# Kernel optimization log

Measured on AMD Instinct MI355X. Metric: run time of the kernel, lower is better.

The kernel has to match this reference:

```python
import jax, jax.numpy as jnp
import numpy as np

G, B, K, D = 16384, 4, 2, 64
NEG = -1e30


def _mlp3(x, w1, b1, w2, b2, w3, b3):
    # MLP: linear->relu x3 (BatchNorm defined but unused in original forward)
    h = jax.nn.relu(x @ w1 + b1)
    h = jax.nn.relu(h @ w2 + b2)
    return jax.nn.relu(h @ w3 + b3)


def setup_inputs() -> dict:
    key = jax.random.key(0)
    ks = jax.random.split(key, 32)

    def lin(k, fan_in, fan_out):
        k1, k2 = jax.random.split(k)
        s = 1.0 / np.sqrt(fan_in)
        w = jax.random.uniform(k1, (fan_in, fan_out), jnp.float32, -s, s)
        b = jax.random.uniform(k2, (fan_out,), jnp.float32, -s, s)
        return w, b

    inp = {}
    inp['ap_feat'] = jax.random.normal(ks[0], (G, B, 1), jnp.float32)
    inp['e_feat'] = jax.random.normal(ks[1], (G, B, K, 2), jnp.float32)
    inp['w_pre_ap'], inp['b_pre_ap'] = lin(ks[2], 1, D)
    inp['w_pre_edge'], inp['b_pre_edge'] = lin(ks[3], 2, D)
    # mlp_update_5 (AP-side neighbor messages), _6 (UE-side), _7 (edge update)
    inp['w5_1'], inp['b5_1'] = lin(ks[4], 2 * D, D)
    inp['w5_2'], inp['b5_2'] = lin(ks[5], D, D)
    inp['w5_3'], inp['b5_3'] = lin(ks[6], D, D)
    inp['w6_1'], inp['b6_1'] = lin(ks[7], 2 * D, D)
    inp['w6_2'], inp['b6_2'] = lin(ks[8], D, D)
    inp['w6_3'], inp['b6_3'] = lin(ks[9], D, D)
    inp['w7_1'], inp['b7_1'] = lin(ks[10], 2 * D, D)
    inp['w7_2'], inp['b7_2'] = lin(ks[11], D, D)
    inp['w7_3'], inp['b7_3'] = lin(ks[12], D, D)
    inp['w_post'], inp['b_post'] = lin(ks[13], D, 2)
    return inp


def _edge_conv(e, a, w5_1, b5_1, w5_2, b5_2, w5_3, b5_3,
               w6_1, b6_1, w6_2, b6_2, w6_3, b6_3,
               w7_1, b7_1, w7_2, b7_2, w7_3, b7_3):
    # e: [G,B,K,D] AP2UE edge hid; a: [G,B,D] AP hid.
    # M1[g,b,j] = mlp5(cat(a[g,b], e[g,b,j])) -- same-AP neighbor edges
    x1 = jnp.concatenate([jnp.broadcast_to(a[:, :, None, :], e.shape), e], axis=-1)  # [G,B,K,2D]
    M1 = _mlp3(x1, w5_1, b5_1, w5_2, b5_2, w5_3, b5_3)  # [G,B,K,D]
    # M2[g,b,bp,k] = mlp6(cat(a[g,b], e[g,bp,k])) -- same-UE neighbor edges
    # (original uses the SRC AP feature here too). Split first linear to
    # avoid materializing the [G,B,B,K,2D] concat.
    h = jax.nn.relu(
        (a @ w6_1[:D])[:, :, None, None, :]
        + (e @ w6_1[D:])[:, None, :, :, :]
        + b6_1)  # [G,B,B,K,D]
    h = jax.nn.relu(h @ w6_2 + b6_2)
    M2 = jax.nn.relu(h @ w6_3 + b6_3)  # [G,B,Bp,K,D]
    # masked max excluding the edge itself
    eyeK = jnp.eye(K, dtype=bool)  # [k, j]
    m1max = jnp.max(jnp.where(eyeK[None, None, :, :, None], NEG,
                              M1[:, :, None, :, :]), axis=3)  # [G,B,K,D]
    eyeB = jnp.eye(B, dtype=bool)  # [b, bp]
    m2max = jnp.max(jnp.where(eyeB[None, :, :, None, None], NEG, M2), axis=2)  # [G,B,K,D]
    agg = jnp.maximum(m1max, m2max)
    # new edge feature: mlp7(cat(agg, e_hid))
    return _mlp3(jnp.concatenate([agg, e], axis=-1),
                 w7_1, b7_1, w7_2, b7_2, w7_3, b7_3)


def reference(ap_feat, e_feat, w_pre_ap, b_pre_ap, w_pre_edge, b_pre_edge,
              w5_1, b5_1, w5_2, b5_2, w5_3, b5_3,
              w6_1, b6_1, w6_2, b6_2, w6_3, b6_3,
              w7_1, b7_1, w7_2, b7_2, w7_3, b7_3,
              w_post, b_post):
    # PreLayer (live branches only: AP nodes and AP2UE edges; APConv/UEConv
    # write node 'new' which is never read, so UE/UE2AP branches are dead).
    a = jax.nn.relu(ap_feat @ w_pre_ap + b_pre_ap)   # [G,B,D]
    e = jax.nn.relu(e_feat @ w_pre_edge + b_pre_edge)  # [G,B,K,D]
    # two UpdateLayers (shared weights: ModuleList([UpdateLayer()]*2) + global MLPs)
    for _ in range(2):
        e = _edge_conv(e, a, w5_1, b5_1, w5_2, b5_2, w5_3, b5_3,
                       w6_1, b6_1, w6_2, b6_2, w6_3, b6_3,
                       w7_1, b7_1, w7_2, b7_2, w7_3, b7_3)
    out = e @ w_post + b_post  # [G,B,K,2]
    r, im = out[..., 0], out[..., 1]
    # norm_func: per-graph [B,K] complex matrix, each row (over K) L2-normalized
    n = jnp.sqrt(jnp.sum(r * r + im * im, axis=-1, keepdims=True))
    return jnp.stack([r / n, im / n], axis=-1)  # [G,B,K,2]
```

## Files before the change

kernel.cpp:

```cpp
#include <hip/hip_runtime.h>


typedef unsigned short u16;
typedef unsigned int   u32;
typedef __attribute__((ext_vector_type(8))) short short8_t;
typedef __attribute__((ext_vector_type(2))) short short2v;
typedef __attribute__((ext_vector_type(4))) float floatx4;

#define LDSFENCE() asm volatile("" ::: "memory")

#define OFF_W51 0
#define OFF_W61 8192
#define OFF_W71 16384
#define OFF_W52 24576
#define OFF_W53 28672
#define OFF_W62 32768
#define OFF_W63 36864
#define OFF_W72 40960
#define OFF_W73 45056
#define WS_U16  49152

#define CB51 0
#define CB52 64
#define CB53 128
#define CB61 192
#define CB62 256
#define CB63 320
#define CB71 384
#define CB72 448
#define CB73 512
#define CWPO 576
#define CBPO 704
#define CWPA 768
#define CBPA 832
#define CWPE 896
#define CBPE 1024
#define CSZ  1088

#define BUF_U16 1088
#define APB_U16 544
#define PW_U16  3264

struct Params {
  const float *ap, *ef;
  const float *wpa, *bpa, *wpe, *bpe;
  const float *w51, *b51, *w52, *b52, *w53, *b53;
  const float *w61, *b61, *w62, *b62, *w63, *b63;
  const float *w71, *b71, *w72, *b72, *w73, *b73;
  const float *wpost, *bpost;
  float *out;
  int gtot;
};

__device__ __forceinline__ u32 pk2(float a, float b) {
  const u32 ua = __float_as_uint(a) + 0x8000u;
  const u32 ub = __float_as_uint(b) + 0x8000u;
  return __builtin_amdgcn_perm(ub, ua, 0x07060302u);
}
__device__ __forceinline__ float blo(u32 v) { return __uint_as_float(v << 16); }
__device__ __forceinline__ float bhi(u32 v) { return __uint_as_float(v & 0xffff0000u); }
__device__ __forceinline__ u32 pkmax(u32 a, u32 b) {
  const short2v r = __builtin_elementwise_max(__builtin_bit_cast(short2v, a),
                                              __builtin_bit_cast(short2v, b));
  return __builtin_bit_cast(u32, r);
}
__device__ __forceinline__ float sel4(int i, float x0, float x1, float x2, float x3) {
  const float lo = (i & 1) ? x1 : x0;
  const float hi = (i & 1) ? x3 : x2;
  return (i & 2) ? hi : lo;
}

__device__ __forceinline__ floatx4 mfma16(short8_t a, short8_t b, floatx4 c) {
  return __builtin_amdgcn_mfma_f32_16x16x32_bf16(a, b, c, 0, 0, 0);
}
__device__ __forceinline__ int rowN(int row) { return row * 8 + (row >> 4) * 8; }
__device__ __forceinline__ short8_t ldN(const u16* buf, int row) {
  const uint4 v = *(const uint4*)(buf + rowN(row));
  return __builtin_bit_cast(short8_t, v);
}
__device__ __forceinline__ uint4 ldN4(const u16* buf, int row) {
  return *(const uint4*)(buf + rowN(row));
}

template<int TSTRIDE>
__device__ __forceinline__ void layerK64R2(floatx4* aX, floatx4* aY,
                                           short8_t x0, short8_t x1,
                                           short8_t y0, short8_t y1,
                                           const u16* B, int l) {
#pragma unroll
  for (int t = 0; t < 4; ++t) {
    const short8_t b0 = *(const short8_t*)(B + (t * TSTRIDE + 0) * 512 + l * 8);
    const short8_t b1 = *(const short8_t*)(B + (t * TSTRIDE + 1) * 512 + l * 8);
    aX[t] = mfma16(x0, b0, aX[t]);
    aY[t] = mfma16(y0, b0, aY[t]);
    aX[t] = mfma16(x1, b1, aX[t]);
    aY[t] = mfma16(y1, b1, aY[t]);
  }
}

__device__ __forceinline__ void layerK128R2(floatx4* aX, floatx4* aY,
                                            const short8_t* fx, const short8_t* fy,
                                            const u16* B, int l) {
#pragma unroll
  for (int t = 0; t < 4; ++t)
#pragma unroll
    for (int h = 0; h < 4; ++h) {
      const short8_t b = *(const short8_t*)(B + (t * 4 + h) * 512 + l * 8);
      aX[t] = mfma16(fx[h], b, aX[t]);
      aY[t] = mfma16(fy[h], b, aY[t]);
    }
}

__device__ __forceinline__ void scatterN_relu(u16* dst, const floatx4* acc, int q, int n) {
  u32* d32 = (u32*)dst;
  const int g = n >> 2, d = n & 3;
#pragma unroll
  for (int tp = 0; tp < 2; ++tp)
#pragma unroll
    for (int r = 0; r < 4; ++r) {
      const int row = tp * 64 + g * 16 + 4 * q + r;
      d32[row * 4 + (row >> 4) * 4 + d] =
          pkmax(pk2(acc[2 * tp + 0][r], acc[2 * tp + 1][r]), 0u);
    }
  LDSFENCE();
}
__device__ __forceinline__ void scatterN_raw(u16* dst, const floatx4* acc, int q, int n) {
  u32* d32 = (u32*)dst;
  const int g = n >> 2, d = n & 3;
#pragma unroll
  for (int tp = 0; tp < 2; ++tp)
#pragma unroll
    for (int r = 0; r < 4; ++r) {
      const int row = tp * 64 + g * 16 + 4 * q + r;
      d32[row * 4 + (row >> 4) * 4 + d] = pk2(acc[2 * tp + 0][r], acc[2 * tp + 1][r]);
    }
  LDSFENCE();
}
__device__ __forceinline__ void scatterN_u32(u16* dst, const u32* v, int q, int n) {
  u32* d32 = (u32*)dst;
  const int g = n >> 2, d = n & 3;
#pragma unroll
  for (int tp = 0; tp < 2; ++tp)
#pragma unroll
    for (int r = 0; r < 4; ++r) {
      const int row = tp * 64 + g * 16 + 4 * q + r;
      d32[row * 4 + (row >> 4) * 4 + d] = v[tp * 4 + r];
    }
  LDSFENCE();
}

__device__ __forceinline__ void scatter_aP(u16* dst, const floatx4* acc, int q, int n,
                                           const float* cb61) {
  u32* d32 = (u32*)dst;
  const int g = n >> 2, d = n & 3;
#pragma unroll
  for (int tp = 0; tp < 2; ++tp) {
    const float bv0 = cb61[32 * tp + n];
    const float bv1 = cb61[32 * tp + 16 + n];
#pragma unroll
    for (int rh = 0; rh < 2; ++rh) {
      const int row = tp * 32 + g * 8 + 2 * q + rh;
      d32[row * 4 + (row >> 4) * 4 + d] =
          pk2(acc[2 * tp + 0][2 * rh] + bv0, acc[2 * tp + 1][2 * rh] + bv1);
    }
  }
  LDSFENCE();
}

__device__ __forceinline__ void init_accL(floatx4* acc, const float* cb, int n) {
#pragma unroll
  for (int t = 0; t < 4; ++t) {
    const float b = cb[16 * t + n];
    floatx4 v; v[0] = b; v[1] = b; v[2] = b; v[3] = b;
    acc[t] = v;
  }
}
__device__ __forceinline__ void init_acc0(floatx4* acc) {
#pragma unroll
  for (int t = 0; t < 4; ++t) { acc[t][0] = 0.f; acc[t][1] = 0.f; acc[t][2] = 0.f; acc[t][3] = 0.f; }
}

struct frag2 { short8_t f0, f1; };

__device__ __forceinline__ frag2 make_a(float apv, int q, const float* sc) {
  frag2 r;
#pragma unroll
  for (int h = 0; h < 2; ++h) {
    const int fb = 32 * h + 8 * q;
    const float4 wa0 = *(const float4*)(sc + CWPA + fb);
    const float4 wa1 = *(const float4*)(sc + CWPA + fb + 4);
    const float4 ba0 = *(const float4*)(sc + CBPA + fb);
    const float4 ba1 = *(const float4*)(sc + CBPA + fb + 4);
    uint4 pa;
    pa.x = pk2(fmaxf(fmaf(apv, wa0.x, ba0.x), 0.f), fmaxf(fmaf(apv, wa0.y, ba0.y), 0.f));
    pa.y = pk2(fmaxf(fmaf(apv, wa0.z, ba0.z), 0.f), fmaxf(fmaf(apv, wa0.w, ba0.w), 0.f));
    pa.z = pk2(fmaxf(fmaf(apv, wa1.x, ba1.x), 0.f), fmaxf(fmaf(apv, wa1.y, ba1.y), 0.f));
    pa.w = pk2(fmaxf(fmaf(apv, wa1.z, ba1.z), 0.f), fmaxf(fmaf(apv, wa1.w, ba1.w), 0.f));
    if (h == 0) r.f0 = __builtin_bit_cast(short8_t, pa);
    else        r.f1 = __builtin_bit_cast(short8_t, pa);
  }
  return r;
}

__device__ __forceinline__ void prelayer(frag2& A, short8_t& e0, short8_t& e1,
                                         const Params& p, const float* sc,
                                         int g0, int q, int n) {
  const float apv = p.ap[(g0 + (n >> 3)) * 4 + ((n >> 1) & 3)];
  A = make_a(apv, q, sc);
  const float f0 = p.ef[(g0 + (n >> 3)) * 16 + (n & 7) * 2];
  const float f1 = p.ef[(g0 + (n >> 3)) * 16 + (n & 7) * 2 + 1];
#pragma unroll
  for (int h = 0; h < 2; ++h) {
    const int fb = 32 * h + 8 * q;
    const float4 w00 = *(const float4*)(sc + CWPE + fb);
    const float4 w01 = *(const float4*)(sc + CWPE + fb + 4);
    const float4 w10 = *(const float4*)(sc + CWPE + 64 + fb);
    const float4 w11 = *(const float4*)(sc + CWPE + 64 + fb + 4);
    const float4 be0 = *(const float4*)(sc + CBPE + fb);
    const float4 be1 = *(const float4*)(sc + CBPE + fb + 4);
    uint4 pe;
    pe.x = pk2(fmaxf(fmaf(f0, w00.x, fmaf(f1, w10.x, be0.x)), 0.f),
               fmaxf(fmaf(f0, w00.y, fmaf(f1, w10.y, be0.y)), 0.f));
    pe.y = pk2(fmaxf(fmaf(f0, w00.z, fmaf(f1, w10.z, be0.z)), 0.f),
               fmaxf(fmaf(f0, w00.w, fmaf(f1, w10.w, be0.w)), 0.f));
    pe.z = pk2(fmaxf(fmaf(f0, w01.x, fmaf(f1, w11.x, be1.x)), 0.f),
               fmaxf(fmaf(f0, w01.y, fmaf(f1, w11.y, be1.y)), 0.f));
    pe.w = pk2(fmaxf(fmaf(f0, w01.z, fmaf(f1, w11.z, be1.z)), 0.f),
               fmaxf(fmaf(f0, w01.w, fmaf(f1, w11.w, be1.w)), 0.f));
    if (h == 0) e0 = __builtin_bit_cast(short8_t, pe);
    else        e1 = __builtin_bit_cast(short8_t, pe);
  }
}

__device__ __forceinline__ void build_h(short8_t* hf0, short8_t* hf1,
                                        const u16* aPb, const u16* BUF,
                                        int q, int n) {
  const int b_ln = (n >> 1) & 3;
  const int ar = 8 * q + (n >> 1);
  const uint4 av0 = ldN4(aPb, ar);
  const uint4 av1 = ldN4(aPb, 32 + ar);
#pragma unroll
  for (int j = 0; j < 3; ++j) {
    const int bp = j + (j >= b_ln);
    const int re = (n & 8) + bp * 2 + (n & 1);
    const uint4 ev0 = ldN4(BUF, 16 * q + re);
    const uint4 ev1 = ldN4(BUF, 64 + 16 * q + re);
    uint4 p0, p1;
    p0.x = pk2(fmaxf(blo(av0.x) + blo(ev0.x), 0.f), fmaxf(bhi(av0.x) + bhi(ev0.x), 0.f));
    p0.y = pk2(fmaxf(blo(av0.y) + blo(ev0.y), 0.f), fmaxf(bhi(av0.y) + bhi(ev0.y), 0.f));
    p0.z = pk2(fmaxf(blo(av0.z) + blo(ev0.z), 0.f), fmaxf(bhi(av0.z) + bhi(ev0.z), 0.f));
    p0.w = pk2(fmaxf(blo(av0.w) + blo(ev0.w), 0.f), fmaxf(bhi(av0.w) + bhi(ev0.w), 0.f));
    p1.x = pk2(fmaxf(blo(av1.x) + blo(ev1.x), 0.f), fmaxf(bhi(av1.x) + bhi(ev1.x), 0.f));
    p1.y = pk2(fmaxf(blo(av1.y) + blo(ev1.y), 0.f), fmaxf(bhi(av1.y) + bhi(ev1.y), 0.f));
    p1.z = pk2(fmaxf(blo(av1.z) + blo(ev1.z), 0.f), fmaxf(bhi(av1.z) + bhi(ev1.z), 0.f));
    p1.w = pk2(fmaxf(blo(av1.w) + blo(ev1.w), 0.f), fmaxf(bhi(av1.w) + bhi(ev1.w), 0.f));
    hf0[j] = __builtin_bit_cast(short8_t, p0);
    hf1[j] = __builtin_bit_cast(short8_t, p1);
  }
}

__device__ __forceinline__ void epilogue(const floatx4* acc3, const float* sc,
                                         float* out, int g0, int q, int n, bool ok) {
  float prr[4] = {0.f, 0.f, 0.f, 0.f}, pii[4] = {0.f, 0.f, 0.f, 0.f};
#pragma unroll
  for (int t = 0; t < 4; ++t) {
    const float wr = sc[CWPO + (16 * t + n) * 2];
    const float wi = sc[CWPO + (16 * t + n) * 2 + 1];
#pragma unroll
    for (int r = 0; r < 4; ++r) {
      const float e = fmaxf(acc3[t][r], 0.f);
      prr[r] = fmaf(e, wr, prr[r]);
      pii[r] = fmaf(e, wi, pii[r]);
    }
  }
  const float bpR = sc[CBPO], bpI = sc[CBPO + 1];
#pragma unroll
  for (int r = 0; r < 4; ++r) {
#pragma unroll
    for (int off = 1; off < 16; off <<= 1) {
      prr[r] += __shfl_xor(prr[r], off, 16);
      pii[r] += __shfl_xor(pii[r], off, 16);
    }
    prr[r] += bpR;
    pii[r] += bpI;
  }
  const int r = n >> 1, c = n & 1, rp = r ^ 1;
  const float pr_r  = sel4(r,  prr[0], prr[1], prr[2], prr[3]);
  const float pi_r  = sel4(r,  pii[0], pii[1], pii[2], pii[3]);
  const float pr_rp = sel4(rp, prr[0], prr[1], prr[2], prr[3]);
  const float pi_rp = sel4(rp, pii[0], pii[1], pii[2], pii[3]);
  const float num = c ? pi_r : pr_r;
  const float n2  = pr_r * pr_r + pi_r * pi_r + pr_rp * pr_rp + pi_rp * pi_rp;
  if (ok && n < 8) out[g0 * 16 + (4 * q + r) * 2 + c] = num / sqrtf(n2);
}

#define NBLK 256
#define NWAVE 8
#define PPW  2

__global__ __launch_bounds__(512, 2)
__attribute__((amdgpu_waves_per_eu(2, 2)))
void hetgnn_mfma(Params p) {
  __shared__ __align__(16) u16   sW[WS_U16];
  __shared__ __align__(16) u16   sAct[NWAVE * PW_U16];
  __shared__ __align__(16) float sConst[CSZ];

  const int tid  = threadIdx.x;
  const int wave = tid >> 6;
  const int l    = tid & 63;
  const int q    = l >> 4;
  const int n    = l & 15;

  {
    for (int fi = wave; fi < 96; fi += NWAVE) {
      int t, h, mi;
      if (fi < 48) { mi = fi >> 4; const int loc = fi & 15; t = loc >> 2; h = loc & 3; }
      else { const int j = fi - 48; mi = 3 + (j >> 3); const int loc = j & 7; t = loc >> 1; h = loc & 1; }
      const float* W =
          (mi == 0) ? p.w51 : (mi == 1) ? p.w61 : (mi == 2) ? p.w71 :
          (mi == 3) ? p.w52 : (mi == 4) ? p.w53 : (mi == 5) ? p.w62 :
          (mi == 6) ? p.w63 : (mi == 7) ? p.w72 : p.w73;
      const int nn = 16 * t + n;
      float w[8];
#pragma unroll
      for (int jj = 0; jj < 8; ++jj) {
        const int kidx = (fi < 48)
            ? 64 * (h >> 1) + 32 * (h & 1) + (jj & 1) * 16 + 4 * q + (jj >> 1)
            : 32 * h + (jj & 1) * 16 + 4 * q + (jj >> 1);
        w[jj] = W[kidx * 64 + nn];
      }
      uint4 o;
      o.x = pk2(w[0], w[1]); o.y = pk2(w[2], w[3]);
      o.z = pk2(w[4], w[5]); o.w = pk2(w[6], w[7]);
      *(uint4*)(sW + fi * 512 + l * 8) = o;
    }
  }
  if (tid < 64) {
    sConst[CB51 + tid] = p.b51[tid];
    sConst[CB52 + tid] = p.b52[tid];
    sConst[CB53 + tid] = p.b53[tid];
    sConst[CB61 + tid] = p.b61[tid];
    sConst[CB62 + tid] = p.b62[tid];
    sConst[CB63 + tid] = p.b63[tid];
    sConst[CB71 + tid] = p.b71[tid];
    sConst[CB72 + tid] = p.b72[tid];
    sConst[CB73 + tid] = p.b73[tid];
    const int feat = 32 * (tid >> 5) + (tid & 1) * 16 + 4 * ((tid >> 3) & 3) + ((tid >> 1) & 3);
    sConst[CWPA + tid] = p.wpa[feat];
    sConst[CBPA + tid] = p.bpa[feat];
    sConst[CBPE + tid] = p.bpe[feat];
  }
  if (tid < 128) {
    sConst[CWPO + tid] = p.wpost[tid];
    const int s = tid & 63;
    const int feat = 32 * (s >> 5) + (s & 1) * 16 + 4 * ((s >> 3) & 3) + ((s >> 1) & 3);
    sConst[CWPE + tid] = p.wpe[(tid >> 6) * 64 + feat];
  }
  if (tid < 2) sConst[CBPO + tid] = p.bpost[tid];
  __syncthreads();

  u16* BUF0 = sAct + wave * PW_U16;
  u16* aPb0 = BUF0 + BUF_U16;
  u16* BUF1 = aPb0 + APB_U16;
  u16* aPb1 = BUF1 + BUF_U16;

  const int wslot = blockIdx.x * NWAVE + wave;

#pragma unroll 1
  for (int pi = 0; pi < PPW; ++pi) {
    const int g0X = (wslot * 4 + 2 * pi) * 2;
    const int g0Y = g0X + 2;
    if (g0X + 2 > p.gtot) break;
    const bool okY = (g0Y + 2 <= p.gtot);
    const int gY  = okY ? g0Y : g0X;

    frag2 AX, AY;
    short8_t ex0, ex1, ey0, ey1;
    prelayer(AX, ex0, ex1, p, sConst, g0X, q, n);
    prelayer(AY, ey0, ey1, p, sConst, gY,  q, n);

    {
      floatx4 aaX[4], aaY[4];
      init_acc0(aaX); init_acc0(aaY);
      layerK64R2<4>(aaX, aaY, AX.f0, AX.f1, AY.f0, AY.f1, sW + OFF_W61, l);
      scatter_aP(aPb0, aaX, q, n, sConst + CB61);
      scatter_aP(aPb1, aaY, q, n, sConst + CB61);
    }

#pragma unroll 1
    for (int it = 0; it < 2; ++it) {
      if (it == 1) {
        ex0 = ldN(BUF0, l); ex1 = ldN(BUF0, 64 + l);
        ey0 = ldN(BUF1, l); ey1 = ldN(BUF1, 64 + l);
      }

      u32 m1pX[8], m1pY[8];
      {
        floatx4 aX[4], aY[4];
        init_accL(aX, sConst + CB51, n); init_accL(aY, sConst + CB51, n);
        const short8_t fx[4] = {AX.f0, AX.f1, ex0, ex1};
        const short8_t fy[4] = {AY.f0, AY.f1, ey0, ey1};
        layerK128R2(aX, aY, fx, fy, sW + OFF_W51, l);
        scatterN_relu(BUF0, aX, q, n);
        scatterN_relu(BUF1, aY, q, n);
        floatx4 bX[4], bY[4];
        init_accL(bX, sConst + CB52, n); init_accL(bY, sConst + CB52, n);
        {
          const short8_t gx0 = ldN(BUF0, l), gx1 = ldN(BUF0, 64 + l);
          const short8_t gy0 = ldN(BUF1, l), gy1 = ldN(BUF1, 64 + l);
          layerK64R2<2>(bX, bY, gx0, gx1, gy0, gy1, sW + OFF_W52, l);
        }
        scatterN_relu(BUF0, bX, q, n);
        scatterN_relu(BUF1, bY, q, n);
        floatx4 cX[4], cY[4];
        init_accL(cX, sConst + CB53, n); init_accL(cY, sConst + CB53, n);
        {
          const short8_t gx0 = ldN(BUF0, l), gx1 = ldN(BUF0, 64 + l);
          const short8_t gy0 = ldN(BUF1, l), gy1 = ldN(BUF1, 64 + l);
          layerK64R2<2>(cX, cY, gx0, gx1, gy0, gy1, sW + OFF_W53, l);
        }
#pragma unroll
        for (int tp = 0; tp < 2; ++tp)
#pragma unroll
          for (int r = 0; r < 4; ++r) {
            m1pX[tp * 4 + r] = pk2(cX[2 * tp][r], cX[2 * tp + 1][r]);
            m1pY[tp * 4 + r] = pk2(cY[2 * tp][r], cY[2 * tp + 1][r]);
          }
      }

      u32 m2pX[8], m2pY[8];
      {
        floatx4 eX[4], eY[4];
        init_acc0(eX); init_acc0(eY);
        layerK64R2<4>(eX, eY, ex0, ex1, ey0, ey1, sW + OFF_W61 + 2 * 512, l);
        scatterN_raw(BUF0, eX, q, n);
        scatterN_raw(BUF1, eY, q, n);

        short8_t hfX0[3], hfX1[3], hfY0[3], hfY1[3];
        build_h(hfX0, hfX1, aPb0, BUF0, q, n);
        build_h(hfY0, hfY1, aPb1, BUF1, q, n);

#pragma unroll
        for (int j = 0; j < 3; ++j) {
          floatx4 uX[4], uY[4];
          init_accL(uX, sConst + CB62, n); init_accL(uY, sConst + CB62, n);
          layerK64R2<2>(uX, uY, hfX0[j], hfX1[j], hfY0[j], hfY1[j], sW + OFF_W62, l);
          scatterN_relu(BUF0, uX, q, n);
          scatterN_relu(BUF1, uY, q, n);
          floatx4 vX[4], vY[4];
          init_accL(vX, sConst + CB63, n); init_accL(vY, sConst + CB63, n);
          {
            const short8_t gx0 = ldN(BUF0, l), gx1 = ldN(BUF0, 64 + l);
            const short8_t gy0 = ldN(BUF1, l), gy1 = ldN(BUF1, 64 + l);
            layerK64R2<2>(vX, vY, gx0, gx1, gy0, gy1, sW + OFF_W63, l);
          }
#pragma unroll
          for (int tp = 0; tp < 2; ++tp)
#pragma unroll
            for (int r = 0; r < 4; ++r) {
              const u32 cXv = pk2(vX[2 * tp][r], vX[2 * tp + 1][r]);
              const u32 cYv = pk2(vY[2 * tp][r], vY[2 * tp + 1][r]);
              const int i = tp * 4 + r;
              m2pX[i] = (j == 0) ? cXv : pkmax(m2pX[i], cXv);
              m2pY[i] = (j == 0) ? cYv : pkmax(m2pY[i], cYv);
            }
        }
      }

      {
        u32 agX[8], agY[8];
#pragma unroll
        for (int tp = 0; tp < 2; ++tp)
#pragma unroll
          for (int r = 0; r < 4; ++r) {
            const int i = tp * 4 + r;
            agX[i] = pkmax(pkmax(m1pX[tp * 4 + (r ^ 1)], m2pX[i]), 0u);
            agY[i] = pkmax(pkmax(m1pY[tp * 4 + (r ^ 1)], m2pY[i]), 0u);
          }
        scatterN_u32(BUF0, agX, q, n);
        scatterN_u32(BUF1, agY, q, n);
        floatx4 aX[4], aY[4];
        init_accL(aX, sConst + CB71, n); init_accL(aY, sConst + CB71, n);
        {
          const short8_t gx0 = ldN(BUF0, l), gx1 = ldN(BUF0, 64 + l);
          const short8_t gy0 = ldN(BUF1, l), gy1 = ldN(BUF1, 64 + l);
          const short8_t fx[4] = {gx0, gx1, ex0, ex1};
          const short8_t fy[4] = {gy0, gy1, ey0, ey1};
          layerK128R2(aX, aY, fx, fy, sW + OFF_W71, l);
        }
        scatterN_relu(BUF0, aX, q, n);
        scatterN_relu(BUF1, aY, q, n);
        floatx4 bX[4], bY[4];
        init_accL(bX, sConst + CB72, n); init_accL(bY, sConst + CB72, n);
        {
          const short8_t gx0 = ldN(BUF0, l), gx1 = ldN(BUF0, 64 + l);
          const short8_t gy0 = ldN(BUF1, l), gy1 = ldN(BUF1, 64 + l);
          layerK64R2<2>(bX, bY, gx0, gx1, gy0, gy1, sW + OFF_W72, l);
        }
        scatterN_relu(BUF0, bX, q, n);
        scatterN_relu(BUF1, bY, q, n);
        floatx4 cX[4], cY[4];
        init_accL(cX, sConst + CB73, n); init_accL(cY, sConst + CB73, n);
        {
          const short8_t gx0 = ldN(BUF0, l), gx1 = ldN(BUF0, 64 + l);
          const short8_t gy0 = ldN(BUF1, l), gy1 = ldN(BUF1, 64 + l);
          layerK64R2<2>(cX, cY, gx0, gx1, gy0, gy1, sW + OFF_W73, l);
        }

        if (it == 0) {
          scatterN_relu(BUF0, cX, q, n);
          scatterN_relu(BUF1, cY, q, n);
        } else {
          epilogue(cX, sConst, p.out, g0X, q, n, true);
          epilogue(cY, sConst, p.out, g0Y, q, n, okY);
        }
      }
    }
  }
}

extern "C" void kernel_launch(void* const* d_in, const int* in_sizes, int n_in,
                              void* d_out, int out_size, void* d_ws, size_t ws_size,
                              hipStream_t stream) {
  Params p;
  p.ap    = (const float*)d_in[0];
  p.ef    = (const float*)d_in[1];
  p.wpa   = (const float*)d_in[2];  p.bpa   = (const float*)d_in[3];
  p.wpe   = (const float*)d_in[4];  p.bpe   = (const float*)d_in[5];
  p.w51   = (const float*)d_in[6];  p.b51   = (const float*)d_in[7];
  p.w52   = (const float*)d_in[8];  p.b52   = (const float*)d_in[9];
  p.w53   = (const float*)d_in[10]; p.b53   = (const float*)d_in[11];
  p.w61   = (const float*)d_in[12]; p.b61   = (const float*)d_in[13];
  p.w62   = (const float*)d_in[14]; p.b62   = (const float*)d_in[15];
  p.w63   = (const float*)d_in[16]; p.b63   = (const float*)d_in[17];
  p.w71   = (const float*)d_in[18]; p.b71   = (const float*)d_in[19];
  p.w72   = (const float*)d_in[20]; p.b72   = (const float*)d_in[21];
  p.w73   = (const float*)d_in[22]; p.b73   = (const float*)d_in[23];
  p.wpost = (const float*)d_in[24]; p.bpost = (const float*)d_in[25];
  p.out   = (float*)d_out;
  p.gtot  = in_sizes[0] / 4;

  hipLaunchKernelGGL(hetgnn_mfma, dim3(NBLK), dim3(512), 0, stream, p);
}
```

Measured before the change: 149.8 us.

## Drop split-linear mlp6 trick and dual-tile interleave for one tile per wave

The wave now handles one 2-graph tile per pass instead of two interleaved X/Y tiles, with four passes per wave instead of two. The precomputed a@W61 and e@W61 halves and the VALU-built relu(a+e) hidden fragments are removed. Each of the three mlp6 neighbours now runs a full K=128 MFMA over the concatenated [a, e_neighbour] read from an LDS edge buffer. This trades more matrix work for less VALU bf16 unpack/add work, fewer live registers and less LDS per wave, but it loses the instruction-level parallelism that two independent tiles gave.

```diff
diff --git a/kernel.cpp b/kernel.cpp
--- a/kernel.cpp
+++ b/kernel.cpp
@@ -38,8 +38,8 @@
 #define CSZ  1088
 
 #define BUF_U16 1088
-#define APB_U16 544
-#define PW_U16  3264
+#define ET_U16  1088
+#define PW_U16  2176
 
 struct Params {
   const float *ap, *ef;
@@ -57,8 +57,6 @@
   const u32 ub = __float_as_uint(b) + 0x8000u;
   return __builtin_amdgcn_perm(ub, ua, 0x07060302u);
 }
-__device__ __forceinline__ float blo(u32 v) { return __uint_as_float(v << 16); }
-__device__ __forceinline__ float bhi(u32 v) { return __uint_as_float(v & 0xffff0000u); }
 __device__ __forceinline__ u32 pkmax(u32 a, u32 b) {
   const short2v r = __builtin_elementwise_max(__builtin_bit_cast(short2v, a),
                                               __builtin_bit_cast(short2v, b));
@@ -78,37 +76,31 @@
   const uint4 v = *(const uint4*)(buf + rowN(row));
   return __builtin_bit_cast(short8_t, v);
 }
-__device__ __forceinline__ uint4 ldN4(const u16* buf, int row) {
-  return *(const uint4*)(buf + rowN(row));
-}
-
-template<int TSTRIDE>
-__device__ __forceinline__ void layerK64R2(floatx4* aX, floatx4* aY,
+__device__ __forceinline__ void writeF(u16* buf, int row, short8_t f) {
+  *(uint4*)(buf + rowN(row)) = __builtin_bit_cast(uint4, f);
+}
+
+template<int TS>
+__device__ __forceinline__ void layerK64R(floatx4* acc, short8_t x0, short8_t x1,
+                                          const u16* B, int l) {
+#pragma unroll
+  for (int t = 0; t < 4; ++t) {
+    const short8_t b0 = *(const short8_t*)(B + (t * TS + 0) * 512 + l * 8);
+    const short8_t b1 = *(const short8_t*)(B + (t * TS + 1) * 512 + l * 8);
+    acc[t] = mfma16(x0, b0, acc[t]);
+    acc[t] = mfma16(x1, b1, acc[t]);
+  }
+}
+__device__ __forceinline__ void layerK128R(floatx4* acc,
                                            short8_t x0, short8_t x1,
-                                           short8_t y0, short8_t y1,
+                                           short8_t x2, short8_t x3,
                                            const u16* B, int l) {
-#pragma unroll
-  for (int t = 0; t < 4; ++t) {
-    const short8_t b0 = *(const short8_t*)(B + (t * TSTRIDE + 0) * 512 + l * 8);
-    const short8_t b1 = *(const short8_t*)(B + (t * TSTRIDE + 1) * 512 + l * 8);
-    aX[t] = mfma16(x0, b0, aX[t]);
-    aY[t] = mfma16(y0, b0, aY[t]);
-    aX[t] = mfma16(x1, b1, aX[t]);
-    aY[t] = mfma16(y1, b1, aY[t]);
-  }
-}
-
-__device__ __forceinline__ void layerK128R2(floatx4* aX, floatx4* aY,
-                                            const short8_t* fx, const short8_t* fy,
-                                            const u16* B, int l) {
+  const short8_t x[4] = {x0, x1, x2, x3};
 #pragma unroll
   for (int t = 0; t < 4; ++t)
 #pragma unroll
-    for (int h = 0; h < 4; ++h) {
-      const short8_t b = *(const short8_t*)(B + (t * 4 + h) * 512 + l * 8);
-      aX[t] = mfma16(fx[h], b, aX[t]);
-      aY[t] = mfma16(fy[h], b, aY[t]);
-    }
+    for (int h = 0; h < 4; ++h)
+      acc[t] = mfma16(x[h], *(const short8_t*)(B + (t * 4 + h) * 512 + l * 8), acc[t]);
 }
 
 __device__ __forceinline__ void scatterN_relu(u16* dst, const floatx4* acc, int q, int n) {
@@ -124,18 +116,6 @@
     }
   LDSFENCE();
 }
-__device__ __forceinline__ void scatterN_raw(u16* dst, const floatx4* acc, int q, int n) {
-  u32* d32 = (u32*)dst;
-  const int g = n >> 2, d = n & 3;
-#pragma unroll
-  for (int tp = 0; tp < 2; ++tp)
-#pragma unroll
-    for (int r = 0; r < 4; ++r) {
-      const int row = tp * 64 + g * 16 + 4 * q + r;
-      d32[row * 4 + (row >> 4) * 4 + d] = pk2(acc[2 * tp + 0][r], acc[2 * tp + 1][r]);
-    }
-  LDSFENCE();
-}
 __device__ __forceinline__ void scatterN_u32(u16* dst, const u32* v, int q, int n) {
   u32* d32 = (u32*)dst;
   const int g = n >> 2, d = n & 3;
@@ -146,24 +126,6 @@
       const int row = tp * 64 + g * 16 + 4 * q + r;
       d32[row * 4 + (row >> 4) * 4 + d] = v[tp * 4 + r];
     }
-  LDSFENCE();
-}
-
-__device__ __forceinline__ void scatter_aP(u16* dst, const floatx4* acc, int q, int n,
-                                           const float* cb61) {
-  u32* d32 = (u32*)dst;
-  const int g = n >> 2, d = n & 3;
-#pragma unroll
-  for (int tp = 0; tp < 2; ++tp) {
-    const float bv0 = cb61[32 * tp + n];
-    const float bv1 = cb61[32 * tp + 16 + n];
-#pragma unroll
-    for (int rh = 0; rh < 2; ++rh) {
-      const int row = tp * 32 + g * 8 + 2 * q + rh;
-      d32[row * 4 + (row >> 4) * 4 + d] =
-          pk2(acc[2 * tp + 0][2 * rh] + bv0, acc[2 * tp + 1][2 * rh] + bv1);
-    }
-  }
   LDSFENCE();
 }
 
@@ -174,10 +136,6 @@
     floatx4 v; v[0] = b; v[1] = b; v[2] = b; v[3] = b;
     acc[t] = v;
   }
-}
-__device__ __forceinline__ void init_acc0(floatx4* acc) {
-#pragma unroll
-  for (int t = 0; t < 4; ++t) { acc[t][0] = 0.f; acc[t][1] = 0.f; acc[t][2] = 0.f; acc[t][3] = 0.f; }
 }
 
 struct frag2 { short8_t f0, f1; };
@@ -232,35 +190,8 @@
   }
 }
 
-__device__ __forceinline__ void build_h(short8_t* hf0, short8_t* hf1,
-                                        const u16* aPb, const u16* BUF,
-                                        int q, int n) {
-  const int b_ln = (n >> 1) & 3;
-  const int ar = 8 * q + (n >> 1);
-  const uint4 av0 = ldN4(aPb, ar);
-  const uint4 av1 = ldN4(aPb, 32 + ar);
-#pragma unroll
-  for (int j = 0; j < 3; ++j) {
-    const int bp = j + (j >= b_ln);
-    const int re = (n & 8) + bp * 2 + (n & 1);
-    const uint4 ev0 = ldN4(BUF, 16 * q + re);
-    const uint4 ev1 = ldN4(BUF, 64 + 16 * q + re);
-    uint4 p0, p1;
-    p0.x = pk2(fmaxf(blo(av0.x) + blo(ev0.x), 0.f), fmaxf(bhi(av0.x) + bhi(ev0.x), 0.f));
-    p0.y = pk2(fmaxf(blo(av0.y) + blo(ev0.y), 0.f), fmaxf(bhi(av0.y) + bhi(ev0.y), 0.f));
-    p0.z = pk2(fmaxf(blo(av0.z) + blo(ev0.z), 0.f), fmaxf(bhi(av0.z) + bhi(ev0.z), 0.f));
-    p0.w = pk2(fmaxf(blo(av0.w) + blo(ev0.w), 0.f), fmaxf(bhi(av0.w) + bhi(ev0.w), 0.f));
-    p1.x = pk2(fmaxf(blo(av1.x) + blo(ev1.x), 0.f), fmaxf(bhi(av1.x) + bhi(ev1.x), 0.f));
-    p1.y = pk2(fmaxf(blo(av1.y) + blo(ev1.y), 0.f), fmaxf(bhi(av1.y) + bhi(ev1.y), 0.f));
-    p1.z = pk2(fmaxf(blo(av1.z) + blo(ev1.z), 0.f), fmaxf(bhi(av1.z) + bhi(ev1.z), 0.f));
-    p1.w = pk2(fmaxf(blo(av1.w) + blo(ev1.w), 0.f), fmaxf(bhi(av1.w) + bhi(ev1.w), 0.f));
-    hf0[j] = __builtin_bit_cast(short8_t, p0);
-    hf1[j] = __builtin_bit_cast(short8_t, p1);
-  }
-}
-
 __device__ __forceinline__ void epilogue(const floatx4* acc3, const float* sc,
-                                         float* out, int g0, int q, int n, bool ok) {
+                                         float* out, int g0, int q, int n) {
   float prr[4] = {0.f, 0.f, 0.f, 0.f}, pii[4] = {0.f, 0.f, 0.f, 0.f};
 #pragma unroll
   for (int t = 0; t < 4; ++t) {
@@ -291,12 +222,12 @@
   const float pi_rp = sel4(rp, pii[0], pii[1], pii[2], pii[3]);
   const float num = c ? pi_r : pr_r;
   const float n2  = pr_r * pr_r + pi_r * pi_r + pr_rp * pr_rp + pi_rp * pi_rp;
-  if (ok && n < 8) out[g0 * 16 + (4 * q + r) * 2 + c] = num / sqrtf(n2);
+  if (n < 8) out[g0 * 16 + (4 * q + r) * 2 + c] = num / sqrtf(n2);
 }
 
 #define NBLK 256
 #define NWAVE 8
-#define PPW  2
+#define PPW  4
 
 __global__ __launch_bounds__(512, 2)
 __attribute__((amdgpu_waves_per_eu(2, 2)))
@@ -359,160 +290,108 @@
   if (tid < 2) sConst[CBPO + tid] = p.bpost[tid];
   __syncthreads();
 
-  u16* BUF0 = sAct + wave * PW_U16;
-  u16* aPb0 = BUF0 + BUF_U16;
-  u16* BUF1 = aPb0 + APB_U16;
-  u16* aPb1 = BUF1 + BUF_U16;
+  u16* BUF = sAct + wave * PW_U16;
+  u16* eT  = BUF + BUF_U16;
+
+  const int b_ln = (n >> 1) & 3;
+  int re[3];
+#pragma unroll
+  for (int j = 0; j < 3; ++j) {
+    const int bp = j + (j >= b_ln);
+    re[j] = 16 * q + (n & 8) + 2 * bp + (n & 1);
+  }
 
   const int wslot = blockIdx.x * NWAVE + wave;
 
 #pragma unroll 1
   for (int pi = 0; pi < PPW; ++pi) {
-    const int g0X = (wslot * 4 + 2 * pi) * 2;
-    const int g0Y = g0X + 2;
-    if (g0X + 2 > p.gtot) break;
-    const bool okY = (g0Y + 2 <= p.gtot);
-    const int gY  = okY ? g0Y : g0X;
-
-    frag2 AX, AY;
-    short8_t ex0, ex1, ey0, ey1;
-    prelayer(AX, ex0, ex1, p, sConst, g0X, q, n);
-    prelayer(AY, ey0, ey1, p, sConst, gY,  q, n);
-
-    {
-      floatx4 aaX[4], aaY[4];
-      init_acc0(aaX); init_acc0(aaY);
-      layerK64R2<4>(aaX, aaY, AX.f0, AX.f1, AY.f0, AY.f1, sW + OFF_W61, l);
-      scatter_aP(aPb0, aaX, q, n, sConst + CB61);
-      scatter_aP(aPb1, aaY, q, n, sConst + CB61);
-    }
+    const int g0 = (wslot * PPW + pi) * 2;
+    if (g0 + 2 > p.gtot) break;
+
+    frag2 A;
+    short8_t e0, e1;
+    prelayer(A, e0, e1, p, sConst, g0, q, n);
 
 #pragma unroll 1
     for (int it = 0; it < 2; ++it) {
       if (it == 1) {
-        ex0 = ldN(BUF0, l); ex1 = ldN(BUF0, 64 + l);
-        ey0 = ldN(BUF1, l); ey1 = ldN(BUF1, 64 + l);
+        e0 = ldN(eT, l); e1 = ldN(eT, 64 + l);
+      } else {
+        writeF(eT, l, e0); writeF(eT, 64 + l, e1);
+        LDSFENCE();
       }
 
-      u32 m1pX[8], m1pY[8];
+      u32 m1p[8];
       {
-        floatx4 aX[4], aY[4];
-        init_accL(aX, sConst + CB51, n); init_accL(aY, sConst + CB51, n);
-        const short8_t fx[4] = {AX.f0, AX.f1, ex0, ex1};
-        const short8_t fy[4] = {AY.f0, AY.f1, ey0, ey1};
-        layerK128R2(aX, aY, fx, fy, sW + OFF_W51, l);
-        scatterN_relu(BUF0, aX, q, n);
-        scatterN_relu(BUF1, aY, q, n);
-        floatx4 bX[4], bY[4];
-        init_accL(bX, sConst + CB52, n); init_accL(bY, sConst + CB52, n);
-        {
-          const short8_t gx0 = ldN(BUF0, l), gx1 = ldN(BUF0, 64 + l);
-          const short8_t gy0 = ldN(BUF1, l), gy1 = ldN(BUF1, 64 + l);
-          layerK64R2<2>(bX, bY, gx0, gx1, gy0, gy1, sW + OFF_W52, l);
-        }
-        scatterN_relu(BUF0, bX, q, n);
-        scatterN_relu(BUF1, bY, q, n);
-        floatx4 cX[4], cY[4];
-        init_accL(cX, sConst + CB53, n); init_accL(cY, sConst + CB53, n);
-        {
-          const short8_t gx0 = ldN(BUF0, l), gx1 = ldN(BUF0, 64 + l);
-          const short8_t gy0 = ldN(BUF1, l), gy1 = ldN(BUF1, 64 + l);
-          layerK64R2<2>(cX, cY, gx0, gx1, gy0, gy1, sW + OFF_W53, l);
-        }
+        floatx4 acc[4];
+        init_accL(acc, sConst + CB51, n);
+        layerK128R(acc, A.f0, A.f1, e0, e1, sW + OFF_W51, l);
+        scatterN_relu(BUF, acc, q, n);
+        short8_t t0 = ldN(BUF, l), t1 = ldN(BUF, 64 + l);
+        init_accL(acc, sConst + CB52, n);
+        layerK64R<2>(acc, t0, t1, sW + OFF_W52, l);
+        scatterN_relu(BUF, acc, q, n);
+        t0 = ldN(BUF, l); t1 = ldN(BUF, 64 + l);
+        init_accL(acc, sConst + CB53, n);
+        layerK64R<2>(acc, t0, t1, sW + OFF_W53, l);
 #pragma unroll
         for (int tp = 0; tp < 2; ++tp)
 #pragma unroll
+          for (int r = 0; r < 4; ++r)
+            m1p[tp * 4 + r] = pk2(acc[2 * tp][r], acc[2 * tp + 1][r]);
+      }
+
+      u32 m2p[8];
+#pragma unroll
+      for (int j = 0; j < 3; ++j) {
+        const short8_t en0 = ldN(eT, re[j]);
+        const short8_t en1 = ldN(eT, 64 + re[j]);
+        floatx4 acc[4];
+        init_accL(acc, sConst + CB61, n);
+        layerK128R(acc, A.f0, A.f1, en0, en1, sW + OFF_W61, l);
+        scatterN_relu(BUF, acc, q, n);
+        short8_t t0 = ldN(BUF, l), t1 = ldN(BUF, 64 + l);
+        init_accL(acc, sConst + CB62, n);
+        layerK64R<2>(acc, t0, t1, sW + OFF_W62, l);
+        scatterN_relu(BUF, acc, q, n);
+        t0 = ldN(BUF, l); t1 = ldN(BUF, 64 + l);
+        init_accL(acc, sConst + CB63, n);
+        layerK64R<2>(acc, t0, t1, sW + OFF_W63, l);
+#pragma unroll
+        for (int tp = 0; tp < 2; ++tp)
+#pragma unroll
           for (int r = 0; r < 4; ++r) {
-            m1pX[tp * 4 + r] = pk2(cX[2 * tp][r], cX[2 * tp + 1][r]);
-            m1pY[tp * 4 + r] = pk2(cY[2 * tp][r], cY[2 * tp + 1][r]);
+            const u32 cv = pk2(acc[2 * tp][r], acc[2 * tp + 1][r]);
+            const int i = tp * 4 + r;
+            m2p[i] = (j == 0) ? cv : pkmax(m2p[i], cv);
           }
       }
 
-      u32 m2pX[8], m2pY[8];
       {
-        floatx4 eX[4], eY[4];
-        init_acc0(eX); init_acc0(eY);
-        layerK64R2<4>(eX, eY, ex0, ex1, ey0, ey1, sW + OFF_W61 + 2 * 512, l);
-        scatterN_raw(BUF0, eX, q, n);
-        scatterN_raw(BUF1, eY, q, n);
-
-        short8_t hfX0[3], hfX1[3], hfY0[3], hfY1[3];
-        build_h(hfX0, hfX1, aPb0, BUF0, q, n);
-        build_h(hfY0, hfY1, aPb1, BUF1, q, n);
-
-#pragma unroll
-        for (int j = 0; j < 3; ++j) {
-          floatx4 uX[4], uY[4];
-          init_accL(uX, sConst + CB62, n); init_accL(uY, sConst + CB62, n);
-          layerK64R2<2>(uX, uY, hfX0[j], hfX1[j], hfY0[j], hfY1[j], sW + OFF_W62, l);
-          scatterN_relu(BUF0, uX, q, n);
-          scatterN_relu(BUF1, uY, q, n);
-          floatx4 vX[4], vY[4];
-          init_accL(vX, sConst + CB63, n); init_accL(vY, sConst + CB63, n);
-          {
-            const short8_t gx0 = ldN(BUF0, l), gx1 = ldN(BUF0, 64 + l);
-            const short8_t gy0 = ldN(BUF1, l), gy1 = ldN(BUF1, 64 + l);
-            layerK64R2<2>(vX, vY, gx0, gx1, gy0, gy1, sW + OFF_W63, l);
-          }
-#pragma unroll
-          for (int tp = 0; tp < 2; ++tp)
-#pragma unroll
-            for (int r = 0; r < 4; ++r) {
-              const u32 cXv = pk2(vX[2 * tp][r], vX[2 * tp + 1][r]);
-              const u32 cYv = pk2(vY[2 * tp][r], vY[2 * tp + 1][r]);
-              const int i = tp * 4 + r;
-              m2pX[i] = (j == 0) ? cXv : pkmax(m2pX[i], cXv);
-              m2pY[i] = (j == 0) ? cYv : pkmax(m2pY[i], cYv);
-            }
-        }
-      }
-
-      {
-        u32 agX[8], agY[8];
+        u32 agp[8];
 #pragma unroll
         for (int tp = 0; tp < 2; ++tp)
 #pragma unroll
-          for (int r = 0; r < 4; ++r) {
-            const int i = tp * 4 + r;
-            agX[i] = pkmax(pkmax(m1pX[tp * 4 + (r ^ 1)], m2pX[i]), 0u);
-            agY[i] = pkmax(pkmax(m1pY[tp * 4 + (r ^ 1)], m2pY[i]), 0u);
-          }
-        scatterN_u32(BUF0, agX, q, n);
-        scatterN_u32(BUF1, agY, q, n);
-        floatx4 aX[4], aY[4];
-        init_accL(aX, sConst + CB71, n); init_accL(aY, sConst + CB71, n);
-        {
-          const short8_t gx0 = ldN(BUF0, l), gx1 = ldN(BUF0, 64 + l);
-          const short8_t gy0 = ldN(BUF1, l), gy1 = ldN(BUF1, 64 + l);
-          const short8_t fx[4] = {gx0, gx1, ex0, ex1};
-          const short8_t fy[4] = {gy0, gy1, ey0, ey1};
-          layerK128R2(aX, aY, fx, fy, sW + OFF_W71, l);
-        }
-        scatterN_relu(BUF0, aX, q, n);
-        scatterN_relu(BUF1, aY, q, n);
-        floatx4 bX[4], bY[4];
-        init_accL(bX, sConst + CB72, n); init_accL(bY, sConst + CB72, n);
-        {
-          const short8_t gx0 = ldN(BUF0, l), gx1 = ldN(BUF0, 64 + l);
-          const short8_t gy0 = ldN(BUF1, l), gy1 = ldN(BUF1, 64 + l);
-          layerK64R2<2>(bX, bY, gx0, gx1, gy0, gy1, sW + OFF_W72, l);
-        }
-        scatterN_relu(BUF0, bX, q, n);
-        scatterN_relu(BUF1, bY, q, n);
-        floatx4 cX[4], cY[4];
-        init_accL(cX, sConst + CB73, n); init_accL(cY, sConst + CB73, n);
-        {
-          const short8_t gx0 = ldN(BUF0, l), gx1 = ldN(BUF0, 64 + l);
-          const short8_t gy0 = ldN(BUF1, l), gy1 = ldN(BUF1, 64 + l);
-          layerK64R2<2>(cX, cY, gx0, gx1, gy0, gy1, sW + OFF_W73, l);
-        }
+          for (int r = 0; r < 4; ++r)
+            agp[tp * 4 + r] = pkmax(pkmax(m1p[tp * 4 + (r ^ 1)], m2p[tp * 4 + r]), 0u);
+        scatterN_u32(BUF, agp, q, n);
+        short8_t g0f = ldN(BUF, l), g1f = ldN(BUF, 64 + l);
+        floatx4 acc[4];
+        init_accL(acc, sConst + CB71, n);
+        layerK128R(acc, g0f, g1f, e0, e1, sW + OFF_W71, l);
+        scatterN_relu(BUF, acc, q, n);
+        g0f = ldN(BUF, l); g1f = ldN(BUF, 64 + l);
+        init_accL(acc, sConst + CB72, n);
+        layerK64R<2>(acc, g0f, g1f, sW + OFF_W72, l);
+        scatterN_relu(BUF, acc, q, n);
+        g0f = ldN(BUF, l); g1f = ldN(BUF, 64 + l);
+        init_accL(acc, sConst + CB73, n);
+        layerK64R<2>(acc, g0f, g1f, sW + OFF_W73, l);
 
         if (it == 0) {
-          scatterN_relu(BUF0, cX, q, n);
-          scatterN_relu(BUF1, cY, q, n);
+          scatterN_relu(eT, acc, q, n);
         } else {
-          epilogue(cX, sConst, p.out, g0X, q, n, true);
-          epilogue(cY, sConst, p.out, g0Y, q, n, okY);
+          epilogue(acc, sConst, p.out, g0, q, n);
         }
       }
     }
```

Measured after the change: 162.2 us. 1.08x slower.

## Replace split first-layer M2 computation with per-neighbor full K128 GEMM via bpermute

Applied to the files above, without the earlier changes.

The old code split mlp6's first linear into an AP part and an edge part, precomputing both and combining them with a bf16 add in LDS (build_h). The new code gathers each neighbor's edge fragments across lanes with ds_bpermute and runs the full 128-wide first layer per neighbor (three times). This drops the per-wave aP LDS buffers, the scatter and build_h passes, and the bf16 rounding of the intermediate sum, which shrinks LDS per wave. In exchange it roughly triples the MFMA work of mlp6's first layer.

```diff
diff --git a/kernel.cpp b/kernel.cpp
--- a/kernel.cpp
+++ b/kernel.cpp
@@ -38,8 +38,7 @@
 #define CSZ  1088
 
 #define BUF_U16 1088
-#define APB_U16 544
-#define PW_U16  3264
+#define PW_U16  2176
 
 struct Params {
   const float *ap, *ef;
@@ -57,8 +56,6 @@
   const u32 ub = __float_as_uint(b) + 0x8000u;
   return __builtin_amdgcn_perm(ub, ua, 0x07060302u);
 }
-__device__ __forceinline__ float blo(u32 v) { return __uint_as_float(v << 16); }
-__device__ __forceinline__ float bhi(u32 v) { return __uint_as_float(v & 0xffff0000u); }
 __device__ __forceinline__ u32 pkmax(u32 a, u32 b) {
   const short2v r = __builtin_elementwise_max(__builtin_bit_cast(short2v, a),
                                               __builtin_bit_cast(short2v, b));
@@ -78,8 +75,14 @@
   const uint4 v = *(const uint4*)(buf + rowN(row));
   return __builtin_bit_cast(short8_t, v);
 }
-__device__ __forceinline__ uint4 ldN4(const u16* buf, int row) {
-  return *(const uint4*)(buf + rowN(row));
+__device__ __forceinline__ short8_t bperm8(int addr, short8_t f) {
+  const uint4 v = __builtin_bit_cast(uint4, f);
+  uint4 r;
+  r.x = (u32)__builtin_amdgcn_ds_bpermute(addr, (int)v.x);
+  r.y = (u32)__builtin_amdgcn_ds_bpermute(addr, (int)v.y);
+  r.z = (u32)__builtin_amdgcn_ds_bpermute(addr, (int)v.z);
+  r.w = (u32)__builtin_amdgcn_ds_bpermute(addr, (int)v.w);
+  return __builtin_bit_cast(short8_t, r);
 }
 
 template<int TSTRIDE>
@@ -124,18 +127,6 @@
     }
   LDSFENCE();
 }
-__device__ __forceinline__ void scatterN_raw(u16* dst, const floatx4* acc, int q, int n) {
-  u32* d32 = (u32*)dst;
-  const int g = n >> 2, d = n & 3;
-#pragma unroll
-  for (int tp = 0; tp < 2; ++tp)
-#pragma unroll
-    for (int r = 0; r < 4; ++r) {
-      const int row = tp * 64 + g * 16 + 4 * q + r;
-      d32[row * 4 + (row >> 4) * 4 + d] = pk2(acc[2 * tp + 0][r], acc[2 * tp + 1][r]);
-    }
-  LDSFENCE();
-}
 __device__ __forceinline__ void scatterN_u32(u16* dst, const u32* v, int q, int n) {
   u32* d32 = (u32*)dst;
   const int g = n >> 2, d = n & 3;
@@ -146,24 +137,6 @@
       const int row = tp * 64 + g * 16 + 4 * q + r;
       d32[row * 4 + (row >> 4) * 4 + d] = v[tp * 4 + r];
     }
-  LDSFENCE();
-}
-
-__device__ __forceinline__ void scatter_aP(u16* dst, const floatx4* acc, int q, int n,
-                                           const float* cb61) {
-  u32* d32 = (u32*)dst;
-  const int g = n >> 2, d = n & 3;
-#pragma unroll
-  for (int tp = 0; tp < 2; ++tp) {
-    const float bv0 = cb61[32 * tp + n];
-    const float bv1 = cb61[32 * tp + 16 + n];
-#pragma unroll
-    for (int rh = 0; rh < 2; ++rh) {
-      const int row = tp * 32 + g * 8 + 2 * q + rh;
-      d32[row * 4 + (row >> 4) * 4 + d] =
-          pk2(acc[2 * tp + 0][2 * rh] + bv0, acc[2 * tp + 1][2 * rh] + bv1);
-    }
-  }
   LDSFENCE();
 }
 
@@ -174,10 +147,6 @@
     floatx4 v; v[0] = b; v[1] = b; v[2] = b; v[3] = b;
     acc[t] = v;
   }
-}
-__device__ __forceinline__ void init_acc0(floatx4* acc) {
-#pragma unroll
-  for (int t = 0; t < 4; ++t) { acc[t][0] = 0.f; acc[t][1] = 0.f; acc[t][2] = 0.f; acc[t][3] = 0.f; }
 }
 
 struct frag2 { short8_t f0, f1; };
@@ -232,33 +201,6 @@
   }
 }
 
-__device__ __forceinline__ void build_h(short8_t* hf0, short8_t* hf1,
-                                        const u16* aPb, const u16* BUF,
-                                        int q, int n) {
-  const int b_ln = (n >> 1) & 3;
-  const int ar = 8 * q + (n >> 1);
-  const uint4 av0 = ldN4(aPb, ar);
-  const uint4 av1 = ldN4(aPb, 32 + ar);
-#pragma unroll
-  for (int j = 0; j < 3; ++j) {
-    const int bp = j + (j >= b_ln);
-    const int re = (n & 8) + bp * 2 + (n & 1);
-    const uint4 ev0 = ldN4(BUF, 16 * q + re);
-    const uint4 ev1 = ldN4(BUF, 64 + 16 * q + re);
-    uint4 p0, p1;
-    p0.x = pk2(fmaxf(blo(av0.x) + blo(ev0.x), 0.f), fmaxf(bhi(av0.x) + bhi(ev0.x), 0.f));
-    p0.y = pk2(fmaxf(blo(av0.y) + blo(ev0.y), 0.f), fmaxf(bhi(av0.y) + bhi(ev0.y), 0.f));
-    p0.z = pk2(fmaxf(blo(av0.z) + blo(ev0.z), 0.f), fmaxf(bhi(av0.z) + bhi(ev0.z), 0.f));
-    p0.w = pk2(fmaxf(blo(av0.w) + blo(ev0.w), 0.f), fmaxf(bhi(av0.w) + bhi(ev0.w), 0.f));
-    p1.x = pk2(fmaxf(blo(av1.x) + blo(ev1.x), 0.f), fmaxf(bhi(av1.x) + bhi(ev1.x), 0.f));
-    p1.y = pk2(fmaxf(blo(av1.y) + blo(ev1.y), 0.f), fmaxf(bhi(av1.y) + bhi(ev1.y), 0.f));
-    p1.z = pk2(fmaxf(blo(av1.z) + blo(ev1.z), 0.f), fmaxf(bhi(av1.z) + bhi(ev1.z), 0.f));
-    p1.w = pk2(fmaxf(blo(av1.w) + blo(ev1.w), 0.f), fmaxf(bhi(av1.w) + bhi(ev1.w), 0.f));
-    hf0[j] = __builtin_bit_cast(short8_t, p0);
-    hf1[j] = __builtin_bit_cast(short8_t, p1);
-  }
-}
-
 __device__ __forceinline__ void epilogue(const floatx4* acc3, const float* sc,
                                          float* out, int g0, int q, int n, bool ok) {
   float prr[4] = {0.f, 0.f, 0.f, 0.f}, pii[4] = {0.f, 0.f, 0.f, 0.f};
@@ -360,9 +302,15 @@
   __syncthreads();
 
   u16* BUF0 = sAct + wave * PW_U16;
-  u16* aPb0 = BUF0 + BUF_U16;
-  u16* BUF1 = aPb0 + APB_U16;
-  u16* aPb1 = BUF1 + BUF_U16;
+  u16* BUF1 = BUF0 + BUF_U16;
+
+  const int b_ln = (n >> 1) & 3;
+  int vnb[3];
+#pragma unroll
+  for (int j = 0; j < 3; ++j) {
+    const int bp = j + (j >= b_ln);
+    vnb[j] = (16 * q + (n & 8) + 2 * bp + (n & 1)) << 2;
+  }
 
   const int wslot = blockIdx.x * NWAVE + wave;
 
@@ -378,14 +326,6 @@
     short8_t ex0, ex1, ey0, ey1;
     prelayer(AX, ex0, ex1, p, sConst, g0X, q, n);
     prelayer(AY, ey0, ey1, p, sConst, gY,  q, n);
-
-    {
-      floatx4 aaX[4], aaY[4];
-      init_acc0(aaX); init_acc0(aaY);
-      layerK64R2<4>(aaX, aaY, AX.f0, AX.f1, AY.f0, AY.f1, sW + OFF_W61, l);
-      scatter_aP(aPb0, aaX, q, n, sConst + CB61);
-      scatter_aP(aPb1, aaY, q, n, sConst + CB61);
-    }
 
 #pragma unroll 1
     for (int it = 0; it < 2; ++it) {
@@ -429,42 +369,47 @@
       }
 
       u32 m2pX[8], m2pY[8];
-      {
-        floatx4 eX[4], eY[4];
-        init_acc0(eX); init_acc0(eY);
-        layerK64R2<4>(eX, eY, ex0, ex1, ey0, ey1, sW + OFF_W61 + 2 * 512, l);
-        scatterN_raw(BUF0, eX, q, n);
-        scatterN_raw(BUF1, eY, q, n);
-
-        short8_t hfX0[3], hfX1[3], hfY0[3], hfY1[3];
-        build_h(hfX0, hfX1, aPb0, BUF0, q, n);
-        build_h(hfY0, hfY1, aPb1, BUF1, q, n);
-
-#pragma unroll
-        for (int j = 0; j < 3; ++j) {
-          floatx4 uX[4], uY[4];
-          init_accL(uX, sConst + CB62, n); init_accL(uY, sConst + CB62, n);
-          layerK64R2<2>(uX, uY, hfX0[j], hfX1[j], hfY0[j], hfY1[j], sW + OFF_W62, l);
-          scatterN_relu(BUF0, uX, q, n);
-          scatterN_relu(BUF1, uY, q, n);
-          floatx4 vX[4], vY[4];
-          init_accL(vX, sConst + CB63, n); init_accL(vY, sConst + CB63, n);
-          {
-            const short8_t gx0 = ldN(BUF0, l), gx1 = ldN(BUF0, 64 + l);
-            const short8_t gy0 = ldN(BUF1, l), gy1 = ldN(BUF1, 64 + l);
-            layerK64R2<2>(vX, vY, gx0, gx1, gy0, gy1, sW + OFF_W63, l);
+#pragma unroll
+      for (int j = 0; j < 3; ++j) {
+        const short8_t enX0 = bperm8(vnb[j], ex0);
+        const short8_t enX1 = bperm8(vnb[j], ex1);
+        const short8_t enY0 = bperm8(vnb[j], ey0);
+        const short8_t enY1 = bperm8(vnb[j], ey1);
+        floatx4 uX[4], uY[4];
+        init_accL(uX, sConst + CB61, n); init_accL(uY, sConst + CB61, n);
+        {
+          const short8_t fx[4] = {AX.f0, AX.f1, enX0, enX1};
+          const short8_t fy[4] = {AY.f0, AY.f1, enY0, enY1};
+          layerK128R2(uX, uY, fx, fy, sW + OFF_W61, l);
+        }
+        scatterN_relu(BUF0, uX, q, n);
+        scatterN_relu(BUF1, uY, q, n);
+        floatx4 vX[4], vY[4];
+        init_accL(vX, sConst + CB62, n); init_accL(vY, sConst + CB62, n);
+        {
+          const short8_t gx0 = ldN(BUF0, l), gx1 = ldN(BUF0, 64 + l);
+          const short8_t gy0 = ldN(BUF1, l), gy1 = ldN(BUF1, 64 + l);
+          layerK64R2<2>(vX, vY, gx0, gx1, gy0, gy1, sW + OFF_W62, l);
+        }
+        scatterN_relu(BUF0, vX, q, n);
+        scatterN_relu(BUF1, vY, q, n);
+        floatx4 wX[4], wY[4];
+        init_accL(wX, sConst + CB63, n); init_accL(wY, sConst + CB63, n);
+        {
+          const short8_t gx0 = ldN(BUF0, l), gx1 = ldN(BUF0, 64 + l);
+          const short8_t gy0 = ldN(BUF1, l), gy1 = ldN(BUF1, 64 + l);
+          layerK64R2<2>(wX, wY, gx0, gx1, gy0, gy1, sW + OFF_W63, l);
+        }
+#pragma unroll
+        for (int tp = 0; tp < 2; ++tp)
+#pragma unroll
+          for (int r = 0; r < 4; ++r) {
+            const u32 cXv = pk2(wX[2 * tp][r], wX[2 * tp + 1][r]);
+            const u32 cYv = pk2(wY[2 * tp][r], wY[2 * tp + 1][r]);
+            const int i = tp * 4 + r;
+            m2pX[i] = (j == 0) ? cXv : pkmax(m2pX[i], cXv);
+            m2pY[i] = (j == 0) ? cYv : pkmax(m2pY[i], cYv);
           }
-#pragma unroll
-          for (int tp = 0; tp < 2; ++tp)
-#pragma unroll
-            for (int r = 0; r < 4; ++r) {
-              const u32 cXv = pk2(vX[2 * tp][r], vX[2 * tp + 1][r]);
-              const u32 cYv = pk2(vY[2 * tp][r], vY[2 * tp + 1][r]);
-              const int i = tp * 4 + r;
-              m2pX[i] = (j == 0) ? cXv : pkmax(m2pX[i], cXv);
-              m2pY[i] = (j == 0) ? cYv : pkmax(m2pY[i], cYv);
-            }
-        }
       }
 
       {
```

New measurement: 155.8 us. +4.0%, slower.
